# Optimization experiments

Measured on AMD Instinct MI355X. Metric: run time of the kernel, lower is better.

Reference implementation:

```python
import jax, jax.numpy as jnp
import numpy as np

T, H, I, E = 2048, 1024, 512, 64            # tokens, hidden, moe_intermediate, n_routed_experts
N_GROUP, TOPK_GROUP, TOP_K = 8, 4, 6


def setup_inputs() -> dict:
    key = jax.random.key(0)
    k = jax.random.split(key, 6)
    hidden_states = jax.random.normal(k[0], (T, H), jnp.float32)
    gate_w = jax.random.normal(k[1], (E, H), jnp.float32) * (H ** -0.5)   # router Linear weight [E, H]
    e_bias = jax.random.normal(k[2], (E,), jnp.float32) * 0.02            # e_score_correction_bias
    w1 = jax.random.normal(k[3], (E, H, I), jnp.float32) * (H ** -0.5)    # gate proj per expert
    w3 = jax.random.normal(k[4], (E, H, I), jnp.float32) * (H ** -0.5)    # up proj per expert
    w2 = jax.random.normal(k[5], (E, I, H), jnp.float32) * (I ** -0.5)    # down proj per expert
    return {"hidden_states": hidden_states, "gate_w": gate_w, "e_bias": e_bias,
            "w1": w1, "w3": w3, "w2": w2}


def _grouped_topk(scores, e_bias):
    # DeepSeek-V3 style node-limited routing with sigmoid scoring + correction bias.
    # scores: [T, E] sigmoid scores. Bias is used ONLY for selection, not for weights.
    sfc = scores + e_bias[None, :]                                 # scores for choice
    grp = sfc.reshape(scores.shape[0], N_GROUP, -1)                # [T, G, E/G]
    grp_scores = jax.lax.top_k(grp, 2)[0].sum(-1)                  # sum of top-2 per group [T, G]
    top_g = jax.lax.top_k(grp_scores, TOPK_GROUP)[1]               # [T, topk_group]
    gmask = jnp.sum(jax.nn.one_hot(top_g, N_GROUP, dtype=jnp.float32), axis=1) > 0
    emask = jnp.repeat(gmask, scores.shape[1] // N_GROUP, axis=1)  # [T, E]
    masked = jnp.where(emask, sfc, -jnp.inf)
    topk_ids = jax.lax.top_k(masked, TOP_K)[1]                     # [T, K]
    topk_w = jnp.take_along_axis(scores, topk_ids, axis=1)         # weights from unbiased scores
    topk_w = topk_w / topk_w.sum(-1, keepdims=True)                # renormalize (norm_topk_prob)
    return topk_w, topk_ids


def _moe(hidden_states, gate_w, e_bias, w1, w3, w2):
    logits = hidden_states.astype(jnp.float32) @ gate_w.T          # router in float32 [T, E]
    scores = jax.nn.sigmoid(logits)
    topk_w, topk_ids = _grouped_topk(scores, e_bias)
    # --- dispatch: sort (token, slot) pairs by expert id, grouped GEMM, combine ---
    flat_ids = topk_ids.reshape(-1)                                # [T*K]
    order = jnp.argsort(flat_ids)                                  # stable sort by expert
    tok = order // TOP_K                                           # source token per sorted row
    group_sizes = jnp.bincount(flat_ids, length=E).astype(jnp.int32)
    x = hidden_states[tok]                                         # [T*K, H] gathered tokens
    gate = jax.lax.ragged_dot(x, w1, group_sizes)                  # grouped GEMM [T*K, I]
    up = jax.lax.ragged_dot(x, w3, group_sizes)
    act = jax.nn.silu(gate) * up                                   # SwiGLU
    out = jax.lax.ragged_dot(act, w2, group_sizes)                 # [T*K, H]
    wts = topk_w.reshape(-1)[order]
    # combine: weighted scatter-add back to token order
    return jnp.zeros_like(hidden_states).at[tok].add(out * wts[:, None])


def reference(hidden_states, gate_w, e_bias, w1, w3, w2):
    return _moe(hidden_states, gate_w, e_bias, w1, w3, w2)
```

## Files before the change

kernel.cpp:

```cpp
#include <hip/hip_runtime.h>
#include <hip/hip_bf16.h>

#define T_TOK 2048
#define H_DIM 1024
#define I_DIM 512
#define E_NUM 64
#define TOPK  6
#define NROWS (T_TOK * TOPK)

typedef __attribute__((ext_vector_type(8))) short bf16x8;
typedef __attribute__((ext_vector_type(4))) float f32x4;

union U4B8 { uint4 u; bf16x8 b; };

__device__ __forceinline__ unsigned int f2bf(float x) {
  unsigned int u = __float_as_uint(x);
  return (u + 0x7fffu + ((u >> 16) & 1u)) >> 16;
}
__device__ __forceinline__ unsigned int pack2bf(float lo, float hi) {
  __hip_bfloat162 h = __float22bfloat162_rn(make_float2(lo, hi));
  return *reinterpret_cast<unsigned int*>(&h);
}

#define LOADF4(dst, p) \
  asm volatile("global_load_dwordx4 %0, %1, off" : "=v"(dst) : "v"(p))

#define WAITVN(N) do { asm volatile("s_waitcnt vmcnt(" #N ")" ::: "memory"); \
  __builtin_amdgcn_sched_barrier(0); } while (0)

#define BAR_LGKM() do { __builtin_amdgcn_sched_barrier(0); \
  asm volatile("s_waitcnt lgkmcnt(0)\n\ts_barrier" ::: "memory"); \
  __builtin_amdgcn_sched_barrier(0); } while (0)

#define BAR_FREE() do { __builtin_amdgcn_sched_barrier(0); \
  asm volatile("s_barrier" ::: "memory"); \
  __builtin_amdgcn_sched_barrier(0); } while (0)

__device__ __forceinline__ void gload_lds16(const void* gsrc, void* ldst) {
  __builtin_amdgcn_global_load_lds(
      (const __attribute__((address_space(1))) unsigned int*)gsrc,
      (__attribute__((address_space(3))) unsigned int*)ldst, 16, 0, 0);
}

__global__ __launch_bounds__(64)
void router_kernel(const float* __restrict__ hs, const float* __restrict__ gw,
                   const float* __restrict__ eb, int* __restrict__ tk_id,
                   float* __restrict__ tk_w, unsigned short* __restrict__ xb)
{
  const int t = blockIdx.x;
  const int lane = threadIdx.x;
  __shared__ float sh[H_DIM];
  const float4* hrow = (const float4*)(hs + (size_t)t * H_DIM);
  float4* sh4 = (float4*)sh;
  for (int i = lane; i < H_DIM / 4; i += 64) sh4[i] = hrow[i];
  __syncthreads();

  {
    uint4* xrow = (uint4*)(xb + (size_t)t * H_DIM);
    #pragma unroll
    for (int f = 0; f < 2; ++f) {
      int i = lane + f * 64;
      float4 a = sh4[i * 2], b = sh4[i * 2 + 1];
      uint4 o;
      o.x = pack2bf(a.x, a.y); o.y = pack2bf(a.z, a.w);
      o.z = pack2bf(b.x, b.y); o.w = pack2bf(b.z, b.w);
      xrow[i] = o;
    }
  }

  const float* w = gw + (size_t)lane * H_DIM;
  float acc = 0.f;
  for (int k = 0; k < H_DIM; k += 4) {
    float4 wv = *(const float4*)(w + k);
    acc += sh[k] * wv.x + sh[k + 1] * wv.y + sh[k + 2] * wv.z + sh[k + 3] * wv.w;
  }
  const float score = 1.f / (1.f + expf(-acc));
  const float sfc = score + eb[lane];

  float m1v = sfc; int m1i = lane;
  #pragma unroll
  for (int d = 1; d < 8; d <<= 1) {
    float ov = __shfl_xor(m1v, d); int oi = __shfl_xor(m1i, d);
    if (ov > m1v || (ov == m1v && oi < m1i)) { m1v = ov; m1i = oi; }
  }
  float v2 = (lane == m1i) ? -INFINITY : sfc;
  #pragma unroll
  for (int d = 1; d < 8; d <<= 1) v2 = fmaxf(v2, __shfl_xor(v2, d));
  const float gscore = m1v + v2;

  const int myg = lane >> 3;
  int rank = 0;
  #pragma unroll
  for (int g = 0; g < 8; ++g) {
    float gs = __shfl(gscore, g * 8);
    if (gs > gscore || (gs == gscore && g < myg)) rank++;
  }
  float mv = (rank < 4) ? sfc : -INFINITY;

  int isel[TOPK]; float wsel[TOPK]; float wsum = 0.f;
  #pragma unroll
  for (int j = 0; j < TOPK; ++j) {
    float av = mv; int ai = lane;
    #pragma unroll
    for (int d = 1; d < 64; d <<= 1) {
      float ov = __shfl_xor(av, d); int oi = __shfl_xor(ai, d);
      if (ov > av || (ov == av && oi < ai)) { av = ov; ai = oi; }
    }
    float wj = __shfl(score, ai);
    isel[j] = ai; wsel[j] = wj; wsum += wj;
    if (lane == ai) mv = -INFINITY;
  }
  if (lane == 0) {
    float inv = 1.f / wsum;
    #pragma unroll
    for (int j = 0; j < TOPK; ++j) {
      tk_id[t * TOPK + j] = isel[j];
      tk_w[t * TOPK + j] = wsel[j] * inv;
    }
  }
}

__global__ __launch_bounds__(1024)
void build_rows_kernel(const int* __restrict__ tk_id, const float* __restrict__ tk_w,
                       int* __restrict__ off, int* __restrict__ row_tok,
                       float* __restrict__ row_wt)
{
  __shared__ int cnt[E_NUM];
  __shared__ int base[E_NUM];
  const int tid = threadIdx.x;
  if (tid < E_NUM) cnt[tid] = 0;
  __syncthreads();
  for (int i = tid; i < NROWS; i += 1024) atomicAdd(&cnt[tk_id[i]], 1);
  __syncthreads();
  if (tid == 0) {
    int s = 0;
    for (int e = 0; e < E_NUM; ++e) { base[e] = s; off[e] = s; s += cnt[e]; }
    off[E_NUM] = s;
  }
  __syncthreads();
  if (tid < E_NUM) cnt[tid] = base[tid];
  __syncthreads();
  for (int i = tid; i < NROWS; i += 1024) {
    int e = tk_id[i];
    int p = atomicAdd(&cnt[e], 1);
    row_tok[p] = i / TOPK;
    row_wt[p] = tk_w[i];
  }
}

__global__ __launch_bounds__(512, 4)
void gemm1_kernel(const unsigned short* __restrict__ xb, const float* __restrict__ w1,
                  const float* __restrict__ w3, const int* __restrict__ off,
                  const int* __restrict__ row_tok, const float* __restrict__ row_wt,
                  unsigned short* __restrict__ act)
{
  const int e = blockIdx.x & 63;
  const int n0 = (blockIdx.x >> 6) * 128;
  const int r0 = off[e];
  const int R = off[e + 1] - r0;
  const int rt = blockIdx.y;
  if (rt * 128 >= R) return;

  __shared__ unsigned short sA2[2][128 * 32];
  __shared__ unsigned int sB1[4 * 128 * 4];
  __shared__ unsigned int sB3[4 * 128 * 4];

  const int tid = threadIdx.x;
  const int lane = tid & 63;
  const int wv = tid >> 6;
  const int wm = wv >> 2, wn = wv & 3;
  const int l15 = lane & 15, lhi = lane >> 4;

  const unsigned short* asrc;
  {
    int ar = wv * 16 + (lane >> 2);
    int g = rt * 128 + ar; if (g >= R) g = R - 1;
    int tok = row_tok[r0 + g];
    int s = lane & 3;
    asrc = xb + (size_t)tok * H_DIM + ((s ^ ((ar ^ (ar >> 2)) & 3)) << 3);
  }

  const int ht = tid & 255;
  const int qk = ht >> 4;
  const int qn = ht & 15;
  const int k0 = qk * 2;
  const int nb = qn * 8;
  const int cB = k0 >> 3;
  const int pr = (k0 >> 1) & 3;
  const float* wp = ((tid < 256) ? w1 : w3) + (size_t)e * H_DIM * I_DIM + n0 + nb;
  char* const sBw = (char*)((tid < 256) ? sB1 : sB3);

  f32x4 acc1[4][2] = {};
  f32x4 acc3[4][2] = {};
  f32x4 fB[4];

  char* const sB1c = (char*)sB1;
  char* const sB3c = (char*)sB3;

  LOADF4(fB[0], wp + (size_t)k0 * I_DIM);
  LOADF4(fB[1], wp + (size_t)k0 * I_DIM + 4);
  LOADF4(fB[2], wp + (size_t)(k0 + 1) * I_DIM);
  LOADF4(fB[3], wp + (size_t)(k0 + 1) * I_DIM + 4);
  gload_lds16(asrc, &sA2[0][(wv * 16) * 32]);

  for (int kt = 0; kt < 32; ++kt) {
    WAITVN(1);
    #pragma unroll
    for (int j = 0; j < 4; ++j) {
      int n = nb + j;
      unsigned int o16 = (unsigned)((cB * 128 + n) << 4) ^ (unsigned)(((n >> 3) & 7) << 4);
      *(unsigned int*)(sBw + o16 + pr * 4) = pack2bf(fB[0][j], fB[2][j]);
    }
    #pragma unroll
    for (int j = 0; j < 4; ++j) {
      int n = nb + 4 + j;
      unsigned int o16 = (unsigned)((cB * 128 + n) << 4) ^ (unsigned)(((n >> 3) & 7) << 4);
      *(unsigned int*)(sBw + o16 + pr * 4) = pack2bf(fB[1][j], fB[3][j]);
    }
    if (kt < 31) {
      const float* bn = wp + (size_t)((kt + 1) * 32 + k0) * I_DIM;
      LOADF4(fB[0], bn);
      LOADF4(fB[1], bn + 4);
      LOADF4(fB[2], bn + I_DIM);
      LOADF4(fB[3], bn + I_DIM + 4);
    }
    if (kt < 31) { WAITVN(4); } else { WAITVN(0); }
    BAR_LGKM();
    if (kt < 31) {
      gload_lds16(asrc + (kt + 1) * 32, &sA2[(kt + 1) & 1][(wv * 16) * 32]);
    }
    const char* sAb = (const char*)&sA2[kt & 1][0];
    __builtin_amdgcn_s_setprio(1);
    {
      bf16x8 af[4];
      #pragma unroll
      for (int mi = 0; mi < 4; ++mi) {
        int m = wm * 64 + mi * 16 + l15;
        U4B8 t; t.u = *(const uint4*)(sAb + m * 64 + ((lhi ^ ((m ^ (m >> 2)) & 3)) << 4));
        af[mi] = t.b;
      }
      #pragma unroll
      for (int ni = 0; ni < 2; ++ni) {
        int n = wn * 32 + ni * 16 + l15;
        unsigned int o = (unsigned)((lhi * 128 + n) << 4) ^ (unsigned)(((n >> 3) & 7) << 4);
        U4B8 t1; t1.u = *(const uint4*)(sB1c + o);
        U4B8 t3; t3.u = *(const uint4*)(sB3c + o);
        #pragma unroll
        for (int mi = 0; mi < 4; ++mi) {
          acc1[mi][ni] = __builtin_amdgcn_mfma_f32_16x16x32_bf16(af[mi], t1.b, acc1[mi][ni], 0, 0, 0);
          acc3[mi][ni] = __builtin_amdgcn_mfma_f32_16x16x32_bf16(af[mi], t3.b, acc3[mi][ni], 0, 0, 0);
        }
      }
    }
    __builtin_amdgcn_s_setprio(0);
    BAR_FREE();
  }

  #pragma unroll
  for (int mi = 0; mi < 4; ++mi) {
    #pragma unroll
    for (int j = 0; j < 4; ++j) {
      int row = wm * 64 + mi * 16 + lhi * 4 + j;
      int rg = rt * 128 + row;
      if (rg < R) {
        float wt = row_wt[r0 + rg];
        size_t rbase = (size_t)(r0 + rg) * I_DIM + n0 + wn * 32;
        #pragma unroll
        for (int ni = 0; ni < 2; ++ni) {
          float g = acc1[mi][ni][j];
          float u = acc3[mi][ni][j];
          float a = g / (1.f + __expf(-g)) * u * wt;
          act[rbase + ni * 16 + l15] = (unsigned short)f2bf(a);
        }
      }
    }
  }
}

__global__ __launch_bounds__(512, 4)
void gemm2_kernel(const unsigned short* __restrict__ act, const float* __restrict__ w2,
                  const int* __restrict__ off, const int* __restrict__ row_tok,
                  float* __restrict__ out)
{
  const int e = blockIdx.x & 63;
  const int n0 = (blockIdx.x >> 6) * 128;
  const int r0 = off[e];
  const int R = off[e + 1] - r0;
  const int rt = blockIdx.y;
  if (rt * 128 >= R) return;

  __shared__ unsigned short sA2[2][128 * 32];
  __shared__ unsigned int sB[4 * 128 * 4];
  __shared__ int s_tok[128];

  const int tid = threadIdx.x;
  if (tid < 128) {
    int r = rt * 128 + tid;
    int rr = (r < R) ? r : (R - 1);
    s_tok[tid] = row_tok[r0 + rr];
  }
  __syncthreads();

  const int lane = tid & 63;
  const int wv = tid >> 6;
  const int wm = wv >> 2, wn = wv & 3;
  const int l15 = lane & 15, lhi = lane >> 4;

  const unsigned short* asrc;
  {
    int ar = wv * 16 + (lane >> 2);
    int g = rt * 128 + ar; if (g >= R) g = R - 1;
    int s = lane & 3;
    asrc = act + (size_t)(r0 + g) * I_DIM + ((s ^ ((ar ^ (ar >> 2)) & 3)) << 3);
  }

  const int qk = tid >> 5;
  const int qn = tid & 31;
  const int k0 = qk * 2;
  const int nb = qn * 4;
  const int cB = k0 >> 3;
  const int pr = (k0 >> 1) & 3;
  const float* w2p = w2 + (size_t)e * I_DIM * H_DIM + n0 + nb;

  f32x4 acc[4][2] = {};
  f32x4 fB[2];

  char* const sBc = (char*)sB;

  LOADF4(fB[0], w2p + (size_t)k0 * H_DIM);
  LOADF4(fB[1], w2p + (size_t)(k0 + 1) * H_DIM);
  gload_lds16(asrc, &sA2[0][(wv * 16) * 32]);

  for (int kt = 0; kt < 16; ++kt) {
    WAITVN(1);
    #pragma unroll
    for (int j = 0; j < 4; ++j) {
      int n = nb + j;
      unsigned int o16 = (unsigned)((cB * 128 + n) << 4) ^ (unsigned)(((n >> 3) & 7) << 4);
      *(unsigned int*)(sBc + o16 + pr * 4) = pack2bf(fB[0][j], fB[1][j]);
    }
    if (kt < 15) {
      const float* bn = w2p + (size_t)((kt + 1) * 32 + k0) * H_DIM;
      LOADF4(fB[0], bn);
      LOADF4(fB[1], bn + H_DIM);
    }
    if (kt < 15) { WAITVN(2); } else { WAITVN(0); }
    BAR_LGKM();
    if (kt < 15) {
      gload_lds16(asrc + (kt + 1) * 32, &sA2[(kt + 1) & 1][(wv * 16) * 32]);
    }
    const char* sAb = (const char*)&sA2[kt & 1][0];
    __builtin_amdgcn_s_setprio(1);
    {
      bf16x8 af[4];
      #pragma unroll
      for (int mi = 0; mi < 4; ++mi) {
        int m = wm * 64 + mi * 16 + l15;
        U4B8 t; t.u = *(const uint4*)(sAb + m * 64 + ((lhi ^ ((m ^ (m >> 2)) & 3)) << 4));
        af[mi] = t.b;
      }
      #pragma unroll
      for (int ni = 0; ni < 2; ++ni) {
        int n = wn * 32 + ni * 16 + l15;
        unsigned int o = (unsigned)((lhi * 128 + n) << 4) ^ (unsigned)(((n >> 3) & 7) << 4);
        U4B8 tb; tb.u = *(const uint4*)(sBc + o);
        #pragma unroll
        for (int mi = 0; mi < 4; ++mi)
          acc[mi][ni] = __builtin_amdgcn_mfma_f32_16x16x32_bf16(af[mi], tb.b, acc[mi][ni], 0, 0, 0);
      }
    }
    __builtin_amdgcn_s_setprio(0);
    BAR_FREE();
  }

  #pragma unroll
  for (int mi = 0; mi < 4; ++mi) {
    #pragma unroll
    for (int j = 0; j < 4; ++j) {
      int row = wm * 64 + mi * 16 + lhi * 4 + j;
      if (rt * 128 + row < R) {
        float* ob = out + (size_t)s_tok[row] * H_DIM + n0 + wn * 32;
        #pragma unroll
        for (int ni = 0; ni < 2; ++ni) {
          atomicAdd(ob + ni * 16 + l15, acc[mi][ni][j]);
        }
      }
    }
  }
}

extern "C" void kernel_launch(void* const* d_in, const int* in_sizes, int n_in,
                              void* d_out, int out_size, void* d_ws, size_t ws_size,
                              hipStream_t stream)
{
  const float* hs = (const float*)d_in[0];
  const float* gw = (const float*)d_in[1];
  const float* eb = (const float*)d_in[2];
  const float* w1 = (const float*)d_in[3];
  const float* w3 = (const float*)d_in[4];
  const float* w2 = (const float*)d_in[5];
  float* out = (float*)d_out;

  char* ws = (char*)d_ws;
  int*   tk_id   = (int*)(ws);
  float* tk_w    = (float*)(ws + 49152);
  int*   off     = (int*)(ws + 98304);
  int*   row_tok = (int*)(ws + 98816);
  float* row_wt  = (float*)(ws + 147968);
  unsigned short* xb  = (unsigned short*)(ws + 197120);
  unsigned short* act = (unsigned short*)(ws + 197120 + 4194304);

  hipMemsetAsync(out, 0, (size_t)T_TOK * H_DIM * sizeof(float), stream);
  hipLaunchKernelGGL(router_kernel, dim3(T_TOK), dim3(64), 0, stream,
                     hs, gw, eb, tk_id, tk_w, xb);
  hipLaunchKernelGGL(build_rows_kernel, dim3(1), dim3(1024), 0, stream,
                     tk_id, tk_w, off, row_tok, row_wt);
  hipLaunchKernelGGL(gemm1_kernel, dim3(4 * E_NUM, 8, 1), dim3(512), 0, stream,
                     xb, w1, w3, off, row_tok, row_wt, act);
  hipLaunchKernelGGL(gemm2_kernel, dim3(8 * E_NUM, 8, 1), dim3(512), 0, stream,
                     act, w2, off, row_tok, out);
}
```

Measured before the change: 262.8 us.

## Replace atomic scatter-add combine with per-slot bf16 output and gather combine

The down-projection GEMM now writes its per-slot results as bf16 rows in sorted order instead of doing fp32 atomicAdds into the output. A new combine kernel uses an inverse permutation built during row construction to gather each token's six slot rows and sum them, which also removes the output memset. Separately, the router now processes two tokens per 128-thread block. The intent is to avoid atomic contention and traffic, at the cost of an extra kernel launch, a 25MB intermediate buffer, and bf16 rounding of the per-expert outputs before summation.

```diff
diff --git a/kernel.cpp b/kernel.cpp
--- a/kernel.cpp
+++ b/kernel.cpp
@@ -42,16 +42,17 @@
       (__attribute__((address_space(3))) unsigned int*)ldst, 16, 0, 0);
 }
 
-__global__ __launch_bounds__(64)
+__global__ __launch_bounds__(128)
 void router_kernel(const float* __restrict__ hs, const float* __restrict__ gw,
                    const float* __restrict__ eb, int* __restrict__ tk_id,
                    float* __restrict__ tk_w, unsigned short* __restrict__ xb)
 {
-  const int t = blockIdx.x;
-  const int lane = threadIdx.x;
-  __shared__ float sh[H_DIM];
+  const int wv = threadIdx.x >> 6;
+  const int lane = threadIdx.x & 63;
+  const int t = blockIdx.x * 2 + wv;
+  __shared__ float sh[2][H_DIM];
   const float4* hrow = (const float4*)(hs + (size_t)t * H_DIM);
-  float4* sh4 = (float4*)sh;
+  float4* sh4 = (float4*)sh[wv];
   for (int i = lane; i < H_DIM / 4; i += 64) sh4[i] = hrow[i];
   __syncthreads();
 
@@ -69,10 +70,11 @@
   }
 
   const float* w = gw + (size_t)lane * H_DIM;
+  const float* shp = sh[wv];
   float acc = 0.f;
   for (int k = 0; k < H_DIM; k += 4) {
-    float4 wv = *(const float4*)(w + k);
-    acc += sh[k] * wv.x + sh[k + 1] * wv.y + sh[k + 2] * wv.z + sh[k + 3] * wv.w;
+    float4 wvv = *(const float4*)(w + k);
+    acc += shp[k] * wvv.x + shp[k + 1] * wvv.y + shp[k + 2] * wvv.z + shp[k + 3] * wvv.w;
   }
   const float score = 1.f / (1.f + expf(-acc));
   const float sfc = score + eb[lane];
@@ -123,7 +125,7 @@
 __global__ __launch_bounds__(1024)
 void build_rows_kernel(const int* __restrict__ tk_id, const float* __restrict__ tk_w,
                        int* __restrict__ off, int* __restrict__ row_tok,
-                       float* __restrict__ row_wt)
+                       float* __restrict__ row_wt, int* __restrict__ inv)
 {
   __shared__ int cnt[E_NUM];
   __shared__ int base[E_NUM];
@@ -145,6 +147,7 @@
     int p = atomicAdd(&cnt[e], 1);
     row_tok[p] = i / TOPK;
     row_wt[p] = tk_w[i];
+    inv[i] = p;
   }
 }
 
@@ -279,8 +282,7 @@
 
 __global__ __launch_bounds__(512, 4)
 void gemm2_kernel(const unsigned short* __restrict__ act, const float* __restrict__ w2,
-                  const int* __restrict__ off, const int* __restrict__ row_tok,
-                  float* __restrict__ out)
+                  const int* __restrict__ off, unsigned short* __restrict__ slot_out)
 {
   const int e = blockIdx.x & 63;
   const int n0 = (blockIdx.x >> 6) * 128;
@@ -291,16 +293,8 @@
 
   __shared__ unsigned short sA2[2][128 * 32];
   __shared__ unsigned int sB[4 * 128 * 4];
-  __shared__ int s_tok[128];
 
   const int tid = threadIdx.x;
-  if (tid < 128) {
-    int r = rt * 128 + tid;
-    int rr = (r < R) ? r : (R - 1);
-    s_tok[tid] = row_tok[r0 + rr];
-  }
-  __syncthreads();
-
   const int lane = tid & 63;
   const int wv = tid >> 6;
   const int wm = wv >> 2, wn = wv & 3;
@@ -378,15 +372,37 @@
     #pragma unroll
     for (int j = 0; j < 4; ++j) {
       int row = wm * 64 + mi * 16 + lhi * 4 + j;
-      if (rt * 128 + row < R) {
-        float* ob = out + (size_t)s_tok[row] * H_DIM + n0 + wn * 32;
+      int rg = rt * 128 + row;
+      if (rg < R) {
+        unsigned short* ob = slot_out + (size_t)(r0 + rg) * H_DIM + n0 + wn * 32;
         #pragma unroll
         for (int ni = 0; ni < 2; ++ni) {
-          atomicAdd(ob + ni * 16 + l15, acc[mi][ni][j]);
+          ob[ni * 16 + l15] = (unsigned short)f2bf(acc[mi][ni][j]);
         }
       }
     }
   }
+}
+
+__global__ __launch_bounds__(256)
+void combine_kernel(const unsigned short* __restrict__ slot_out,
+                    const int* __restrict__ inv, float* __restrict__ out)
+{
+  const int t = blockIdx.x;
+  const int c = threadIdx.x;
+  int rows[TOPK];
+  #pragma unroll
+  for (int j = 0; j < TOPK; ++j) rows[j] = inv[t * TOPK + j];
+  float a0 = 0.f, a1 = 0.f, a2 = 0.f, a3 = 0.f;
+  #pragma unroll
+  for (int j = 0; j < TOPK; ++j) {
+    const ushort4 v = *(const ushort4*)(slot_out + (size_t)rows[j] * H_DIM + c * 4);
+    a0 += __uint_as_float((unsigned)v.x << 16);
+    a1 += __uint_as_float((unsigned)v.y << 16);
+    a2 += __uint_as_float((unsigned)v.z << 16);
+    a3 += __uint_as_float((unsigned)v.w << 16);
+  }
+  *(float4*)(out + (size_t)t * H_DIM + c * 4) = make_float4(a0, a1, a2, a3);
 }
 
 extern "C" void kernel_launch(void* const* d_in, const int* in_sizes, int n_in,
@@ -407,16 +423,19 @@
   int*   off     = (int*)(ws + 98304);
   int*   row_tok = (int*)(ws + 98816);
   float* row_wt  = (float*)(ws + 147968);
-  unsigned short* xb  = (unsigned short*)(ws + 197120);
-  unsigned short* act = (unsigned short*)(ws + 197120 + 4194304);
-
-  hipMemsetAsync(out, 0, (size_t)T_TOK * H_DIM * sizeof(float), stream);
-  hipLaunchKernelGGL(router_kernel, dim3(T_TOK), dim3(64), 0, stream,
+  int*   inv     = (int*)(ws + 197120);
+  unsigned short* xb  = (unsigned short*)(ws + 246272);
+  unsigned short* act = (unsigned short*)(ws + 246272 + 4194304);
+  unsigned short* slot_out = (unsigned short*)(ws + 246272 + 4194304 + 12582912);
+
+  hipLaunchKernelGGL(router_kernel, dim3(T_TOK / 2), dim3(128), 0, stream,
                      hs, gw, eb, tk_id, tk_w, xb);
   hipLaunchKernelGGL(build_rows_kernel, dim3(1), dim3(1024), 0, stream,
-                     tk_id, tk_w, off, row_tok, row_wt);
+                     tk_id, tk_w, off, row_tok, row_wt, inv);
   hipLaunchKernelGGL(gemm1_kernel, dim3(4 * E_NUM, 8, 1), dim3(512), 0, stream,
                      xb, w1, w3, off, row_tok, row_wt, act);
   hipLaunchKernelGGL(gemm2_kernel, dim3(8 * E_NUM, 8, 1), dim3(512), 0, stream,
-                     act, w2, off, row_tok, out);
-}
+                     act, w2, off, slot_out);
+  hipLaunchKernelGGL(combine_kernel, dim3(T_TOK), dim3(256), 0, stream,
+                     slot_out, inv, out);
+}
```

After: 242.0 us (median of 2 runs). 7.9% less time.
